# Optimization experiments

Measured on AMD Instinct MI355X. Metric: run time of the kernel, lower is better.

Reference implementation:

```python
import jax, jax.numpy as jnp
import numpy as np

EPS = 1e-8


def setup_inputs() -> dict:
    key = jax.random.key(0)
    ks = jax.random.split(key, 6)
    B, N, d, h = 8, 1024, 512, 512
    features = jax.random.normal(ks[0], (B, N, d), dtype=jnp.float32)
    states_mask = jax.random.randint(ks[1], (B, N), 0, 2, dtype=jnp.int32)
    # nn.Linear params (W stored [out, in], y = x @ W.T + b)
    s1 = 1.0 / np.sqrt(d)
    W1 = jax.random.uniform(ks[2], (h, d), jnp.float32, -s1, s1)
    b1 = jax.random.uniform(ks[3], (h,), jnp.float32, -s1, s1)
    s2 = 1.0 / np.sqrt(3 * h)
    W2 = jax.random.uniform(ks[4], (h, 3 * h), jnp.float32, -s2, s2)
    b2 = jax.random.uniform(ks[5], (h,), jnp.float32, -s2, s2)
    return {"features": features, "states_mask": states_mask,
            "W1": W1, "b1": b1, "W2": W2, "b2": b2}


def reference(features, states_mask, W1, b1, W2, b2):
    B, N, d = features.shape
    # score: project_weight(features) @ features^T  -> [B, N, N]
    proj = features @ W1.T + b1
    weight = jnp.einsum('bid,bjd->bij', proj, features)
    sm = states_mask.astype(jnp.float32)
    mask = sm[:, :, None] * sm[:, None, :]              # [B,N,N]
    tri_past = jnp.tril(jnp.ones((N, N), jnp.float32), k=-1)
    tri_fut = jnp.triu(jnp.ones((N, N), jnp.float32), k=1)
    past_mask = tri_past[None] * mask
    future_mask = tri_fut[None] * mask
    past_w = weight * past_mask
    past_w = past_w / (past_mask.sum(axis=2, keepdims=True) + EPS)
    fut_w = weight * future_mask
    fut_w = fut_w / (future_mask.sum(axis=2, keepdims=True) + EPS)
    # weighted sums: equivalent to the repeated-feature reduction, without O(N^2 d) memory
    past_features = jnp.einsum('bij,bjd->bid', past_w, features)
    future_features = jnp.einsum('bij,bjd->bid', fut_w, features)
    context = jnp.concatenate((past_features, features, future_features), axis=-1)
    context = context @ W2.T + b2
    return context
```

## Files before the change

kernel.cpp:

```cpp
#include <hip/hip_runtime.h>


constexpr int BATCH = 8;
constexpr int SEQ   = 1024;
constexpr int DIM   = 512;
constexpr int HID   = 512;

typedef __bf16 bf16_t;
typedef bf16_t bf16x8 __attribute__((ext_vector_type(8)));
typedef float  f32x4  __attribute__((ext_vector_type(4)));
typedef float  f4     __attribute__((ext_vector_type(4)));

typedef __attribute__((address_space(1))) void gv_t;
typedef __attribute__((address_space(3))) void lv_t;

__device__ __forceinline__ void gload16(const bf16_t* g, bf16_t* l) {
  __builtin_amdgcn_global_load_lds((gv_t*)g, (lv_t*)l, 16, 0, 0);
}

#define WAIT3() asm volatile("s_waitcnt vmcnt(3)" ::: "memory")
#define WAIT0() asm volatile("s_waitcnt vmcnt(0)" ::: "memory")
#define BAR()   { __builtin_amdgcn_s_barrier(); __builtin_amdgcn_sched_barrier(0); }

template <int ROWS>
__device__ __forceinline__ void stage(const bf16_t* g, int ld, bf16_t* lds,
                                      int w, int lane) {
  const int r0 = lane >> 2;
  const int kc = ((((lane & 3) - (lane >> 3)) & 3)) * 8;
#pragma unroll
  for (int i = 0; i < ROWS / 64; ++i) {
    const int s = w * (ROWS / 64) + i;
    gload16(g + (size_t)(s * 16 + r0) * ld + kc, lds + s * 512);
  }
}

__device__ __forceinline__ int swz8(int fr, int c0) {
  return (((fr << 2) | ((c0 + (fr >> 1)) & 3)) << 3);
}

__global__ __launch_bounds__(1024) void scales_kernel(
    const int* __restrict__ smask, float* __restrict__ sp, float* __restrict__ sf) {
  const int b = blockIdx.x, t = threadIdx.x;
  const int v = smask[b * SEQ + t];
  int x = v;
#pragma unroll
  for (int o = 1; o < 64; o <<= 1) {
    int y = __shfl_up(x, o, 64);
    if ((t & 63) >= o) x += y;
  }
  __shared__ int wsum[16], wpre[17];
  if ((t & 63) == 63) wsum[t >> 6] = x;
  __syncthreads();
  if (t == 0) { int c = 0; for (int w = 0; w < 16; ++w) { wpre[w] = c; c += wsum[w]; } wpre[16] = c; }
  __syncthreads();
  const int inc = x + wpre[t >> 6];
  const float P  = (float)(inc - v);
  const float Fu = (float)(wpre[16] - inc);
  sp[b * SEQ + t] = v ? 1.f / (P  + 1e-8f) : 0.f;
  sf[b * SEQ + t] = v ? 1.f / (Fu + 1e-8f) : 0.f;
}

__global__ void cvt_kernel(const float* __restrict__ in, bf16_t* __restrict__ out, int n8) {
  const int i = blockIdx.x * blockDim.x + threadIdx.x;
  if (i >= n8) return;
  const f4* p = (const f4*)(in + (size_t)i * 8);
  f4 v0 = p[0], v1 = p[1];
  bf16x8 o;
  o[0] = (bf16_t)v0[0]; o[1] = (bf16_t)v0[1]; o[2] = (bf16_t)v0[2]; o[3] = (bf16_t)v0[3];
  o[4] = (bf16_t)v1[0]; o[5] = (bf16_t)v1[1]; o[6] = (bf16_t)v1[2]; o[7] = (bf16_t)v1[3];
  *(bf16x8*)(out + (size_t)i * 8) = o;
}

__global__ __launch_bounds__(256) void prepw_kernel(
    const float* __restrict__ W1, const float* __restrict__ W2,
    bf16_t* __restrict__ Wpg, bf16_t* __restrict__ W2ac) {
  const int idx = blockIdx.x * 256 + threadIdx.x;
  const int r = idx >> 6, c8 = (idx & 63) * 8;
  const float* src;
  bf16_t* dst;
  if (r < 512)        { src = W1 + (size_t)r * 512 + c8;                    dst = Wpg  + (size_t)r * 512 + c8; }
  else if (r < 1024)  { src = W2 + (size_t)(r - 512) * 1536 + 512 + c8;     dst = Wpg  + (size_t)r * 512 + c8; }
  else if (r < 1536)  { src = W2 + (size_t)(r - 1024) * 1536 + c8;          dst = W2ac + (size_t)(r - 1024) * 512 + c8; }
  else                { src = W2 + (size_t)(r - 1536) * 1536 + 1024 + c8;   dst = W2ac + (size_t)(r - 1024) * 512 + c8; }
  f4 v0 = *(const f4*)src, v1 = *(const f4*)(src + 4);
  bf16x8 o;
  o[0] = (bf16_t)v0[0]; o[1] = (bf16_t)v0[1]; o[2] = (bf16_t)v0[2]; o[3] = (bf16_t)v0[3];
  o[4] = (bf16_t)v1[0]; o[5] = (bf16_t)v1[1]; o[6] = (bf16_t)v1[2]; o[7] = (bf16_t)v1[3];
  *(bf16x8*)dst = o;
}

__device__ __forceinline__ void gemm_ring(
    const bf16_t* __restrict__ A, int lda, const bf16_t* __restrict__ Bt, int ldb,
    int K, bf16_t* As, bf16_t* Bs, f32x4 acc[4][2],
    int w, int lane, int qoff, int mw, int nw) {
  const int NT = K / 32;
  stage<128>(A,       lda, As,        w, lane);
  stage<64>(Bt,       ldb, Bs,        w, lane);
  stage<128>(A + 32,  lda, As + 4096, w, lane);
  stage<64>(Bt + 32,  ldb, Bs + 2048, w, lane);
  WAIT3();
  BAR();
  int cur = 0;
  for (int k = 0; k < NT; ++k) {
    if (k + 2 < NT) {
      const int nx = (cur >= 1) ? cur - 1 : 2;
      stage<128>(A  + (k + 2) * 32, lda, As + nx * 4096, w, lane);
      stage<64>(Bt + (k + 2) * 32, ldb, Bs + nx * 2048, w, lane);
    }
    const bf16_t* ab = As + cur * 4096 + (mw >> 4) * 512 + qoff;
    const bf16_t* bb = Bs + cur * 2048 + (nw >> 4) * 512 + qoff;
    bf16x8 a[4], b[2];
#pragma unroll
    for (int s = 0; s < 4; ++s) a[s] = *(const bf16x8*)&ab[s * 512];
#pragma unroll
    for (int t = 0; t < 2; ++t) b[t] = *(const bf16x8*)&bb[t * 512];
#pragma unroll
    for (int s = 0; s < 4; ++s)
#pragma unroll
      for (int t = 0; t < 2; ++t)
        acc[s][t] = __builtin_amdgcn_mfma_f32_16x16x32_bf16(a[s], b[t], acc[s][t], 0, 0, 0);
    if (k + 1 < NT) {
      if (k + 2 < NT) { WAIT3(); } else { WAIT0(); }
      BAR();
    }
    cur = (cur == 2) ? 0 : cur + 1;
  }
}

#define TILE_IDS                                  \
  const int tid = threadIdx.x;                    \
  const int w = tid >> 6, lane = tid & 63;        \
  const int fr = lane & 15;                       \
  const int qoff = swz8(fr, lane >> 4);           \
  const int mw = (w >> 1) * 64, nw = (w & 1) * 32;\
  const int cr = (lane >> 4) * 4, cc = lane & 15;

__global__ __launch_bounds__(256) void pg_mfma(
    const bf16_t* __restrict__ Fbf, const bf16_t* __restrict__ Wpg,
    const float* __restrict__ b1, const float* __restrict__ b2,
    bf16_t* __restrict__ projbf, float* __restrict__ out) {
  __shared__ bf16_t As[3 * 4096], Bs[3 * 2048];
  TILE_IDS
  const int m0 = blockIdx.y * 128, n0 = blockIdx.x * 64;
  f32x4 acc[4][2] = {};
  gemm_ring(Fbf + (size_t)m0 * DIM, DIM, Wpg + (size_t)n0 * DIM, DIM, DIM,
            As, Bs, acc, w, lane, qoff, mw, nw);
  if (n0 < 512) {
#pragma unroll
    for (int s = 0; s < 4; ++s)
#pragma unroll
      for (int t = 0; t < 2; ++t) {
        const int col = n0 + nw + t * 16 + cc;
        const float bv = b1[col];
#pragma unroll
        for (int r = 0; r < 4; ++r)
          projbf[(size_t)(m0 + mw + s * 16 + cr + r) * HID + col] = (bf16_t)(acc[s][t][r] + bv);
      }
  } else {
#pragma unroll
    for (int s = 0; s < 4; ++s)
#pragma unroll
      for (int t = 0; t < 2; ++t) {
        const int col = (n0 - 512) + nw + t * 16 + cc;
        const float bv = b2[col];
#pragma unroll
        for (int r = 0; r < 4; ++r)
          out[(size_t)(m0 + mw + s * 16 + cr + r) * HID + col] = acc[s][t][r] + bv;
      }
  }
}

__global__ __launch_bounds__(256) void weight_mfma(
    const bf16_t* __restrict__ projbf, const bf16_t* __restrict__ Fbf,
    bf16_t* __restrict__ wbuf, int b0) {
  __shared__ bf16_t As[3 * 4096], Bs[3 * 2048];
  TILE_IDS
  const int b = b0 + blockIdx.z;
  const bf16_t* A  = projbf + (size_t)b * SEQ * DIM;
  const bf16_t* Bt = Fbf    + (size_t)b * SEQ * DIM;
  bf16_t* C = wbuf + (size_t)blockIdx.z * SEQ * SEQ;
  const int m0 = blockIdx.y * 128, n0 = blockIdx.x * 64;
  f32x4 acc[4][2] = {};
  gemm_ring(A + (size_t)m0 * DIM, DIM, Bt + (size_t)n0 * DIM, DIM, DIM,
            As, Bs, acc, w, lane, qoff, mw, nw);
#pragma unroll
  for (int s = 0; s < 4; ++s)
#pragma unroll
    for (int t = 0; t < 2; ++t)
#pragma unroll
      for (int r = 0; r < 4; ++r)
        C[(size_t)(m0 + mw + s * 16 + cr + r) * SEQ + n0 + nw + t * 16 + cc] = (bf16_t)acc[s][t][r];
}

__global__ __launch_bounds__(256) void gact_mfma(
    const bf16_t* __restrict__ W2ac, const bf16_t* __restrict__ Fbf,
    const int* __restrict__ smask, bf16_t* __restrict__ GacT) {
  __shared__ bf16_t As[3 * 4096], Bs[3 * 2048];
  TILE_IDS
  const int b = blockIdx.z;
  const bf16_t* Bt = Fbf + (size_t)b * SEQ * DIM;
  const int m0 = blockIdx.y * 128, n0 = blockIdx.x * 64;
  f32x4 acc[4][2] = {};
  gemm_ring(W2ac + (size_t)m0 * DIM, DIM, Bt + (size_t)n0 * DIM, DIM, DIM,
            As, Bs, acc, w, lane, qoff, mw, nw);
  bf16_t* C = GacT + (size_t)b * SEQ * SEQ;
#pragma unroll
  for (int s = 0; s < 4; ++s)
#pragma unroll
    for (int t = 0; t < 2; ++t) {
      const int j = n0 + nw + t * 16 + cc;
      const float smj = (float)smask[b * SEQ + j];
#pragma unroll
      for (int r = 0; r < 4; ++r)
        C[(size_t)(m0 + mw + s * 16 + cr + r) * SEQ + j] = (bf16_t)(acc[s][t][r] * smj);
    }
}

__global__ __launch_bounds__(256) void tri_mfma(
    const bf16_t* __restrict__ wbuf, const bf16_t* __restrict__ GacT,
    const float* __restrict__ scaleP, const float* __restrict__ scaleF,
    float* __restrict__ out, int b0) {
  __shared__ bf16_t As[3 * 2048], BPs[3 * 2048], BFs[3 * 2048];
  const int tid = threadIdx.x;
  const int w = tid >> 6, lane = tid & 63;
  const int fr = lane & 15, fk = (lane >> 4) * 8;
  const int qoff = swz8(fr, lane >> 4);
  const int mw = (w >> 1) * 32, nw2 = (w & 1) * 32;
  const int cr = (lane >> 4) * 4, cc = lane & 15;
  const int b = b0 + blockIdx.z;
  const bf16_t* A    = wbuf + (size_t)blockIdx.z * SEQ * SEQ;
  const bf16_t* GaTp = GacT + (size_t)b * SEQ * SEQ + (size_t)(blockIdx.x * 64) * SEQ;
  const bf16_t* GaTf = GaTp + (size_t)512 * SEQ;
  const int i0 = blockIdx.y * 64;
  f32x4 accP[2][2] = {}, accF[2][2] = {};
  const bf16_t* Arow = A + (size_t)i0 * SEQ;
  stage<64>(Arow,      SEQ, As,         w, lane);
  stage<64>(GaTp,      SEQ, BPs,        w, lane);
  stage<64>(GaTf,      SEQ, BFs,        w, lane);
  stage<64>(Arow + 32, SEQ, As + 2048,  w, lane);
  stage<64>(GaTp + 32, SEQ, BPs + 2048, w, lane);
  stage<64>(GaTf + 32, SEQ, BFs + 2048, w, lane);
  WAIT3();
  BAR();
  int cur = 0;
  const int NT = SEQ / 32;
  for (int kt = 0; kt < NT; ++kt) {
    const int j0 = kt * 32;
    if (kt + 2 < NT) {
      const int nx = (cur >= 1) ? cur - 1 : 2;
      const int jn = j0 + 64;
      stage<64>(Arow + jn, SEQ, As  + nx * 2048, w, lane);
      stage<64>(GaTp + jn, SEQ, BPs + nx * 2048, w, lane);
      stage<64>(GaTf + jn, SEQ, BFs + nx * 2048, w, lane);
    }
    const bool wP = (j0 < i0 + mw + 31);
    const bool wF = (j0 + 31 > i0 + mw);
    if (wP || wF) {
      const bf16_t* abase  = As  + cur * 2048 + (mw >> 4) * 512 + qoff;
      const bf16_t* bpbase = BPs + cur * 2048 + (nw2 >> 4) * 512 + qoff;
      const bf16_t* bfbase = BFs + cur * 2048 + (nw2 >> 4) * 512 + qoff;
      bf16x8 bP[2], bF[2];
#pragma unroll
      for (int t = 0; t < 2; ++t) {
        if (wP) bP[t] = *(const bf16x8*)&bpbase[t * 512];
        if (wF) bF[t] = *(const bf16x8*)&bfbase[t * 512];
      }
#pragma unroll
      for (int s = 0; s < 2; ++s) {
        const int rlo = i0 + mw + s * 16;
        const bool pAny = (j0 < rlo + 15), pFull = (j0 + 31 < rlo);
        const bool fAny = (j0 + 31 > rlo), fFull = (j0 > rlo + 15);
        if (!pAny && !fAny) continue;
        const bf16x8 a = *(const bf16x8*)&abase[s * 512];
        if (pFull) {
#pragma unroll
          for (int t = 0; t < 2; ++t)
            accP[s][t] = __builtin_amdgcn_mfma_f32_16x16x32_bf16(a, bP[t], accP[s][t], 0, 0, 0);
        } else if (pAny) {
          const int cut = (rlo + fr) - (j0 + fk);
          bf16x8 ap = a;
#pragma unroll
          for (int e = 0; e < 8; ++e) if (e >= cut) ap[e] = (bf16_t)0.f;
#pragma unroll
          for (int t = 0; t < 2; ++t)
            accP[s][t] = __builtin_amdgcn_mfma_f32_16x16x32_bf16(ap, bP[t], accP[s][t], 0, 0, 0);
        }
        if (fFull) {
#pragma unroll
          for (int t = 0; t < 2; ++t)
            accF[s][t] = __builtin_amdgcn_mfma_f32_16x16x32_bf16(a, bF[t], accF[s][t], 0, 0, 0);
        } else if (fAny) {
          const int cut = (rlo + fr) - (j0 + fk);
          bf16x8 af = a;
#pragma unroll
          for (int e = 0; e < 8; ++e) if (e <= cut) af[e] = (bf16_t)0.f;
#pragma unroll
          for (int t = 0; t < 2; ++t)
            accF[s][t] = __builtin_amdgcn_mfma_f32_16x16x32_bf16(af, bF[t], accF[s][t], 0, 0, 0);
        }
      }
    }
    if (kt + 1 < NT) {
      if (kt + 2 < NT) { WAIT3(); } else { WAIT0(); }
      BAR();
    }
    cur = (cur == 2) ? 0 : cur + 1;
  }
#pragma unroll
  for (int s = 0; s < 2; ++s)
#pragma unroll
    for (int r = 0; r < 4; ++r) {
      const int row = i0 + mw + s * 16 + cr + r;
      const float spv = scaleP[b * SEQ + row];
      const float sfv = scaleF[b * SEQ + row];
#pragma unroll
      for (int t = 0; t < 2; ++t) {
        const int col = blockIdx.x * 64 + nw2 + t * 16 + cc;
        const size_t oi = ((size_t)b * SEQ + row) * HID + col;
        out[oi] = accP[s][t][r] * spv + accF[s][t][r] * sfv + out[oi];
      }
    }
}

extern "C" void kernel_launch(void* const* d_in, const int* in_sizes, int n_in,
                              void* d_out, int out_size, void* d_ws, size_t ws_size,
                              hipStream_t stream) {
  const float* F  = (const float*)d_in[0];
  const int*   sm = (const int*)  d_in[1];
  const float* W1 = (const float*)d_in[2];
  const float* b1 = (const float*)d_in[3];
  const float* W2 = (const float*)d_in[4];
  const float* b2 = (const float*)d_in[5];
  float* out = (float*)d_out;

  char* ws = (char*)d_ws;
  size_t off = 0;
  auto take = [&](size_t bytes) -> void* {
    void* p = ws + off;
    off += (bytes + 255) & ~(size_t)255;
    return p;
  };
  bf16_t* Fbf    = (bf16_t*)take((size_t)BATCH * SEQ * DIM * 2);
  bf16_t* projbf = (bf16_t*)take((size_t)BATCH * SEQ * HID * 2);
  bf16_t* GacT   = (bf16_t*)take((size_t)BATCH * SEQ * SEQ * 2);
  bf16_t* Wpg    = (bf16_t*)take((size_t)1024 * 512 * 2);
  bf16_t* W2ac   = (bf16_t*)take((size_t)1024 * 512 * 2);
  float*  scaleP = (float*) take((size_t)BATCH * SEQ * 4);
  float*  scaleF = (float*) take((size_t)BATCH * SEQ * 4);

  const size_t wbytes = (size_t)SEQ * SEQ * 2;
  int chunk = (ws_size > off) ? (int)((ws_size - off) / wbytes) : 1;
  if (chunk > BATCH) chunk = BATCH;
  if (chunk < 1) chunk = 1;
  bf16_t* wbuf = (bf16_t*)(ws + off);

  scales_kernel<<<dim3(BATCH), dim3(1024), 0, stream>>>(sm, scaleP, scaleF);
  cvt_kernel<<<dim3(BATCH * SEQ * DIM / 8 / 256), dim3(256), 0, stream>>>(F, Fbf, BATCH * SEQ * DIM / 8);
  prepw_kernel<<<dim3(512), dim3(256), 0, stream>>>(W1, W2, Wpg, W2ac);

  pg_mfma<<<dim3(1024 / 64, BATCH * SEQ / 128), dim3(256), 0, stream>>>(
      Fbf, Wpg, b1, b2, projbf, out);
  gact_mfma<<<dim3(SEQ / 64, SEQ / 128, BATCH), dim3(256), 0, stream>>>(
      W2ac, Fbf, sm, GacT);
  for (int b0 = 0; b0 < BATCH; b0 += chunk) {
    const int nb = (BATCH - b0 < chunk) ? (BATCH - b0) : chunk;
    weight_mfma<<<dim3(SEQ / 64, SEQ / 128, nb), dim3(256), 0, stream>>>(projbf, Fbf, wbuf, b0);
    tri_mfma<<<dim3(HID / 64, SEQ / 64, nb), dim3(256), 0, stream>>>(
        wbuf, GacT, scaleP, scaleF, out, b0);
  }
}
```

Before: 107.3 us.

## Merge prep and projection kernels, deepen LDS ring to four stages

New measurement: 121.4 us (median of 2 runs). +13.2%, slower.

```diff
diff --git a/kernel.cpp b/kernel.cpp
--- a/kernel.cpp
+++ b/kernel.cpp
@@ -18,6 +18,7 @@
   __builtin_amdgcn_global_load_lds((gv_t*)g, (lv_t*)l, 16, 0, 0);
 }
 
+#define WAIT6() asm volatile("s_waitcnt vmcnt(6)" ::: "memory")
 #define WAIT3() asm volatile("s_waitcnt vmcnt(3)" ::: "memory")
 #define WAIT0() asm volatile("s_waitcnt vmcnt(0)" ::: "memory")
 #define BAR()   { __builtin_amdgcn_s_barrier(); __builtin_amdgcn_sched_barrier(0); }
@@ -38,55 +39,67 @@
   return (((fr << 2) | ((c0 + (fr >> 1)) & 3)) << 3);
 }
 
-__global__ __launch_bounds__(1024) void scales_kernel(
-    const int* __restrict__ smask, float* __restrict__ sp, float* __restrict__ sf) {
-  const int b = blockIdx.x, t = threadIdx.x;
-  const int v = smask[b * SEQ + t];
-  int x = v;
+__global__ __launch_bounds__(256) void prep_kernel(
+    const float* __restrict__ F, const int* __restrict__ smask,
+    const float* __restrict__ W1, const float* __restrict__ W2,
+    bf16_t* __restrict__ Fbf, bf16_t* __restrict__ Wpg, bf16_t* __restrict__ W2ac,
+    float* __restrict__ sp, float* __restrict__ sf) {
+  const int bid = blockIdx.x, tid = threadIdx.x;
+  if (bid < 2048) {
+    const int i = bid * 256 + tid;
+    const f4* p = (const f4*)(F + (size_t)i * 8);
+    f4 v0 = p[0], v1 = p[1];
+    bf16x8 o;
+    o[0] = (bf16_t)v0[0]; o[1] = (bf16_t)v0[1]; o[2] = (bf16_t)v0[2]; o[3] = (bf16_t)v0[3];
+    o[4] = (bf16_t)v1[0]; o[5] = (bf16_t)v1[1]; o[6] = (bf16_t)v1[2]; o[7] = (bf16_t)v1[3];
+    *(bf16x8*)(Fbf + (size_t)i * 8) = o;
+    return;
+  }
+  if (bid < 2560) {
+    const int idx = (bid - 2048) * 256 + tid;
+    const int r = idx >> 6, c8 = (idx & 63) * 8;
+    const float* src;
+    bf16_t* dst;
+    if (r < 512)       { src = W1 + (size_t)r * 512 + c8;                  dst = Wpg  + (size_t)r * 512 + c8; }
+    else if (r < 1024) { src = W2 + (size_t)(r - 512) * 1536 + 512 + c8;   dst = Wpg  + (size_t)r * 512 + c8; }
+    else if (r < 1536) { src = W2 + (size_t)(r - 1024) * 1536 + c8;        dst = W2ac + (size_t)(r - 1024) * 512 + c8; }
+    else               { src = W2 + (size_t)(r - 1536) * 1536 + 1024 + c8; dst = W2ac + (size_t)(r - 1024) * 512 + c8; }
+    f4 v0 = *(const f4*)src, v1 = *(const f4*)(src + 4);
+    bf16x8 o;
+    o[0] = (bf16_t)v0[0]; o[1] = (bf16_t)v0[1]; o[2] = (bf16_t)v0[2]; o[3] = (bf16_t)v0[3];
+    o[4] = (bf16_t)v1[0]; o[5] = (bf16_t)v1[1]; o[6] = (bf16_t)v1[2]; o[7] = (bf16_t)v1[3];
+    *(bf16x8*)dst = o;
+    return;
+  }
+  const int b = bid - 2560;
+  const int4 v4 = ((const int4*)(smask + b * SEQ))[tid];
+  const int tsum = v4.x + v4.y + v4.z + v4.w;
+  int x = tsum;
 #pragma unroll
   for (int o = 1; o < 64; o <<= 1) {
     int y = __shfl_up(x, o, 64);
-    if ((t & 63) >= o) x += y;
-  }
-  __shared__ int wsum[16], wpre[17];
-  if ((t & 63) == 63) wsum[t >> 6] = x;
+    if ((tid & 63) >= o) x += y;
+  }
+  __shared__ int wsum[4], wpre[5];
+  if ((tid & 63) == 63) wsum[tid >> 6] = x;
   __syncthreads();
-  if (t == 0) { int c = 0; for (int w = 0; w < 16; ++w) { wpre[w] = c; c += wsum[w]; } wpre[16] = c; }
+  if (tid == 0) { int c = 0; for (int w = 0; w < 4; ++w) { wpre[w] = c; c += wsum[w]; } wpre[4] = c; }
   __syncthreads();
-  const int inc = x + wpre[t >> 6];
-  const float P  = (float)(inc - v);
-  const float Fu = (float)(wpre[16] - inc);
-  sp[b * SEQ + t] = v ? 1.f / (P  + 1e-8f) : 0.f;
-  sf[b * SEQ + t] = v ? 1.f / (Fu + 1e-8f) : 0.f;
-}
-
-__global__ void cvt_kernel(const float* __restrict__ in, bf16_t* __restrict__ out, int n8) {
-  const int i = blockIdx.x * blockDim.x + threadIdx.x;
-  if (i >= n8) return;
-  const f4* p = (const f4*)(in + (size_t)i * 8);
-  f4 v0 = p[0], v1 = p[1];
-  bf16x8 o;
-  o[0] = (bf16_t)v0[0]; o[1] = (bf16_t)v0[1]; o[2] = (bf16_t)v0[2]; o[3] = (bf16_t)v0[3];
-  o[4] = (bf16_t)v1[0]; o[5] = (bf16_t)v1[1]; o[6] = (bf16_t)v1[2]; o[7] = (bf16_t)v1[3];
-  *(bf16x8*)(out + (size_t)i * 8) = o;
-}
-
-__global__ __launch_bounds__(256) void prepw_kernel(
-    const float* __restrict__ W1, const float* __restrict__ W2,
-    bf16_t* __restrict__ Wpg, bf16_t* __restrict__ W2ac) {
-  const int idx = blockIdx.x * 256 + threadIdx.x;
-  const int r = idx >> 6, c8 = (idx & 63) * 8;
-  const float* src;
-  bf16_t* dst;
-  if (r < 512)        { src = W1 + (size_t)r * 512 + c8;                    dst = Wpg  + (size_t)r * 512 + c8; }
-  else if (r < 1024)  { src = W2 + (size_t)(r - 512) * 1536 + 512 + c8;     dst = Wpg  + (size_t)r * 512 + c8; }
-  else if (r < 1536)  { src = W2 + (size_t)(r - 1024) * 1536 + c8;          dst = W2ac + (size_t)(r - 1024) * 512 + c8; }
-  else                { src = W2 + (size_t)(r - 1536) * 1536 + 1024 + c8;   dst = W2ac + (size_t)(r - 1024) * 512 + c8; }
-  f4 v0 = *(const f4*)src, v1 = *(const f4*)(src + 4);
-  bf16x8 o;
-  o[0] = (bf16_t)v0[0]; o[1] = (bf16_t)v0[1]; o[2] = (bf16_t)v0[2]; o[3] = (bf16_t)v0[3];
-  o[4] = (bf16_t)v1[0]; o[5] = (bf16_t)v1[1]; o[6] = (bf16_t)v1[2]; o[7] = (bf16_t)v1[3];
-  *(bf16x8*)dst = o;
+  const int excl = (x - tsum) + wpre[tid >> 6];
+  const float tot = (float)wpre[4];
+  f4 spv, sfv;
+  int pre = excl;
+  const int e[4] = {v4.x, v4.y, v4.z, v4.w};
+#pragma unroll
+  for (int i = 0; i < 4; ++i) {
+    const float P  = (float)pre;
+    const float Fu = tot - (float)pre - (float)e[i];
+    spv[i] = e[i] ? 1.f / (P  + 1e-8f) : 0.f;
+    sfv[i] = e[i] ? 1.f / (Fu + 1e-8f) : 0.f;
+    pre += e[i];
+  }
+  ((f4*)(sp + b * SEQ))[tid] = spv;
+  ((f4*)(sf + b * SEQ))[tid] = sfv;
 }
 
 __device__ __forceinline__ void gemm_ring(
@@ -94,18 +107,19 @@
     int K, bf16_t* As, bf16_t* Bs, f32x4 acc[4][2],
     int w, int lane, int qoff, int mw, int nw) {
   const int NT = K / 32;
-  stage<128>(A,       lda, As,        w, lane);
-  stage<64>(Bt,       ldb, Bs,        w, lane);
-  stage<128>(A + 32,  lda, As + 4096, w, lane);
-  stage<64>(Bt + 32,  ldb, Bs + 2048, w, lane);
-  WAIT3();
+#pragma unroll
+  for (int p = 0; p < 3; ++p) {
+    stage<128>(A + p * 32, lda, As + p * 4096, w, lane);
+    stage<64>(Bt + p * 32, ldb, Bs + p * 2048, w, lane);
+  }
+  WAIT6();
   BAR();
-  int cur = 0;
   for (int k = 0; k < NT; ++k) {
-    if (k + 2 < NT) {
-      const int nx = (cur >= 1) ? cur - 1 : 2;
-      stage<128>(A  + (k + 2) * 32, lda, As + nx * 4096, w, lane);
-      stage<64>(Bt + (k + 2) * 32, ldb, Bs + nx * 2048, w, lane);
+    const int cur = k & 3;
+    if (k + 3 < NT) {
+      const int nx = (k + 3) & 3;
+      stage<128>(A  + (k + 3) * 32, lda, As + nx * 4096, w, lane);
+      stage<64>(Bt + (k + 3) * 32, ldb, Bs + nx * 2048, w, lane);
     }
     const bf16_t* ab = As + cur * 4096 + (mw >> 4) * 512 + qoff;
     const bf16_t* bb = Bs + cur * 2048 + (nw >> 4) * 512 + qoff;
@@ -119,53 +133,71 @@
 #pragma unroll
       for (int t = 0; t < 2; ++t)
         acc[s][t] = __builtin_amdgcn_mfma_f32_16x16x32_bf16(a[s], b[t], acc[s][t], 0, 0, 0);
-    if (k + 1 < NT) {
-      if (k + 2 < NT) { WAIT3(); } else { WAIT0(); }
-      BAR();
-    }
-    cur = (cur == 2) ? 0 : cur + 1;
-  }
-}
-
-#define TILE_IDS                                  \
-  const int tid = threadIdx.x;                    \
-  const int w = tid >> 6, lane = tid & 63;        \
-  const int fr = lane & 15;                       \
-  const int qoff = swz8(fr, lane >> 4);           \
-  const int mw = (w >> 1) * 64, nw = (w & 1) * 32;\
+    if (k + 3 < NT)      { WAIT6(); BAR(); }
+    else if (k + 2 < NT) { WAIT3(); BAR(); }
+    else if (k + 1 < NT) { WAIT0(); BAR(); }
+  }
+}
+
+__global__ __launch_bounds__(256) void pgga_mfma(
+    const bf16_t* __restrict__ Fbf, const bf16_t* __restrict__ Wpg,
+    const bf16_t* __restrict__ W2ac, const int* __restrict__ smask,
+    const float* __restrict__ b1, const float* __restrict__ b2,
+    bf16_t* __restrict__ projbf, float* __restrict__ out,
+    bf16_t* __restrict__ GacT) {
+  __shared__ bf16_t As[4 * 4096], Bs[4 * 2048];
+  const int tid = threadIdx.x;
+  const int w = tid >> 6, lane = tid & 63;
+  const int fr = lane & 15;
+  const int qoff = swz8(fr, lane >> 4);
+  const int mw = (w >> 1) * 64, nw = (w & 1) * 32;
   const int cr = (lane >> 4) * 4, cc = lane & 15;
-
-__global__ __launch_bounds__(256) void pg_mfma(
-    const bf16_t* __restrict__ Fbf, const bf16_t* __restrict__ Wpg,
-    const float* __restrict__ b1, const float* __restrict__ b2,
-    bf16_t* __restrict__ projbf, float* __restrict__ out) {
-  __shared__ bf16_t As[3 * 4096], Bs[3 * 2048];
-  TILE_IDS
-  const int m0 = blockIdx.y * 128, n0 = blockIdx.x * 64;
+  const int bid = blockIdx.x;
   f32x4 acc[4][2] = {};
-  gemm_ring(Fbf + (size_t)m0 * DIM, DIM, Wpg + (size_t)n0 * DIM, DIM, DIM,
-            As, Bs, acc, w, lane, qoff, mw, nw);
-  if (n0 < 512) {
+  if (bid < 1024) {
+    const int m0 = (bid >> 4) * 128, n0 = (bid & 15) * 64;
+    gemm_ring(Fbf + (size_t)m0 * DIM, DIM, Wpg + (size_t)n0 * DIM, DIM, DIM,
+              As, Bs, acc, w, lane, qoff, mw, nw);
+    if (n0 < 512) {
+#pragma unroll
+      for (int s = 0; s < 4; ++s)
+#pragma unroll
+        for (int t = 0; t < 2; ++t) {
+          const int col = n0 + nw + t * 16 + cc;
+          const float bv = b1[col];
+#pragma unroll
+          for (int r = 0; r < 4; ++r)
+            projbf[(size_t)(m0 + mw + s * 16 + cr + r) * HID + col] = (bf16_t)(acc[s][t][r] + bv);
+        }
+    } else {
+#pragma unroll
+      for (int s = 0; s < 4; ++s)
+#pragma unroll
+        for (int t = 0; t < 2; ++t) {
+          const int col = (n0 - 512) + nw + t * 16 + cc;
+          const float bv = b2[col];
+#pragma unroll
+          for (int r = 0; r < 4; ++r)
+            out[(size_t)(m0 + mw + s * 16 + cr + r) * HID + col] = acc[s][t][r] + bv;
+        }
+    }
+  } else {
+    const int q = bid - 1024;
+    const int b = q >> 7, r7 = q & 127;
+    const int m0 = (r7 >> 4) * 128, n0 = (r7 & 15) * 64;
+    const bf16_t* Bt = Fbf + (size_t)b * SEQ * DIM;
+    gemm_ring(W2ac + (size_t)m0 * DIM, DIM, Bt + (size_t)n0 * DIM, DIM, DIM,
+              As, Bs, acc, w, lane, qoff, mw, nw);
+    bf16_t* C = GacT + (size_t)b * SEQ * SEQ;
 #pragma unroll
     for (int s = 0; s < 4; ++s)
 #pragma unroll
       for (int t = 0; t < 2; ++t) {
-        const int col = n0 + nw + t * 16 + cc;
-        const float bv = b1[col];
+        const int j = n0 + nw + t * 16 + cc;
+        const float smj = (float)smask[b * SEQ + j];
 #pragma unroll
         for (int r = 0; r < 4; ++r)
-          projbf[(size_t)(m0 + mw + s * 16 + cr + r) * HID + col] = (bf16_t)(acc[s][t][r] + bv);
-      }
-  } else {
-#pragma unroll
-    for (int s = 0; s < 4; ++s)
-#pragma unroll
-      for (int t = 0; t < 2; ++t) {
-        const int col = (n0 - 512) + nw + t * 16 + cc;
-        const float bv = b2[col];
-#pragma unroll
-        for (int r = 0; r < 4; ++r)
-          out[(size_t)(m0 + mw + s * 16 + cr + r) * HID + col] = acc[s][t][r] + bv;
+          C[(size_t)(m0 + mw + s * 16 + cr + r) * SEQ + j] = (bf16_t)(acc[s][t][r] * smj);
       }
   }
 }
@@ -173,8 +205,13 @@
 __global__ __launch_bounds__(256) void weight_mfma(
     const bf16_t* __restrict__ projbf, const bf16_t* __restrict__ Fbf,
     bf16_t* __restrict__ wbuf, int b0) {
-  __shared__ bf16_t As[3 * 4096], Bs[3 * 2048];
-  TILE_IDS
+  __shared__ bf16_t As[4 * 4096], Bs[4 * 2048];
+  const int tid = threadIdx.x;
+  const int w = tid >> 6, lane = tid & 63;
+  const int fr = lane & 15;
+  const int qoff = swz8(fr, lane >> 4);
+  const int mw = (w >> 1) * 64, nw = (w & 1) * 32;
+  const int cr = (lane >> 4) * 4, cc = lane & 15;
   const int b = b0 + blockIdx.z;
   const bf16_t* A  = projbf + (size_t)b * SEQ * DIM;
   const bf16_t* Bt = Fbf    + (size_t)b * SEQ * DIM;
@@ -192,35 +229,11 @@
         C[(size_t)(m0 + mw + s * 16 + cr + r) * SEQ + n0 + nw + t * 16 + cc] = (bf16_t)acc[s][t][r];
 }
 
-__global__ __launch_bounds__(256) void gact_mfma(
-    const bf16_t* __restrict__ W2ac, const bf16_t* __restrict__ Fbf,
-    const int* __restrict__ smask, bf16_t* __restrict__ GacT) {
-  __shared__ bf16_t As[3 * 4096], Bs[3 * 2048];
-  TILE_IDS
-  const int b = blockIdx.z;
-  const bf16_t* Bt = Fbf + (size_t)b * SEQ * DIM;
-  const int m0 = blockIdx.y * 128, n0 = blockIdx.x * 64;
-  f32x4 acc[4][2] = {};
-  gemm_ring(W2ac + (size_t)m0 * DIM, DIM, Bt + (size_t)n0 * DIM, DIM, DIM,
-            As, Bs, acc, w, lane, qoff, mw, nw);
-  bf16_t* C = GacT + (size_t)b * SEQ * SEQ;
-#pragma unroll
-  for (int s = 0; s < 4; ++s)
-#pragma unroll
-    for (int t = 0; t < 2; ++t) {
-      const int j = n0 + nw + t * 16 + cc;
-      const float smj = (float)smask[b * SEQ + j];
-#pragma unroll
-      for (int r = 0; r < 4; ++r)
-        C[(size_t)(m0 + mw + s * 16 + cr + r) * SEQ + j] = (bf16_t)(acc[s][t][r] * smj);
-    }
-}
-
 __global__ __launch_bounds__(256) void tri_mfma(
     const bf16_t* __restrict__ wbuf, const bf16_t* __restrict__ GacT,
     const float* __restrict__ scaleP, const float* __restrict__ scaleF,
     float* __restrict__ out, int b0) {
-  __shared__ bf16_t As[3 * 2048], BPs[3 * 2048], BFs[3 * 2048];
+  __shared__ bf16_t As[4 * 2048], BPs[4 * 2048], BFs[4 * 2048];
   const int tid = threadIdx.x;
   const int w = tid >> 6, lane = tid & 63;
   const int fr = lane & 15, fk = (lane >> 4) * 8;
@@ -234,21 +247,21 @@
   const int i0 = blockIdx.y * 64;
   f32x4 accP[2][2] = {}, accF[2][2] = {};
   const bf16_t* Arow = A + (size_t)i0 * SEQ;
-  stage<64>(Arow,      SEQ, As,         w, lane);
-  stage<64>(GaTp,      SEQ, BPs,        w, lane);
-  stage<64>(GaTf,      SEQ, BFs,        w, lane);
-  stage<64>(Arow + 32, SEQ, As + 2048,  w, lane);
-  stage<64>(GaTp + 32, SEQ, BPs + 2048, w, lane);
-  stage<64>(GaTf + 32, SEQ, BFs + 2048, w, lane);
-  WAIT3();
+#pragma unroll
+  for (int p = 0; p < 3; ++p) {
+    stage<64>(Arow + p * 32, SEQ, As  + p * 2048, w, lane);
+    stage<64>(GaTp + p * 32, SEQ, BPs + p * 2048, w, lane);
+    stage<64>(GaTf + p * 32, SEQ, BFs + p * 2048, w, lane);
+  }
+  WAIT6();
   BAR();
-  int cur = 0;
   const int NT = SEQ / 32;
   for (int kt = 0; kt < NT; ++kt) {
     const int j0 = kt * 32;
-    if (kt + 2 < NT) {
-      const int nx = (cur >= 1) ? cur - 1 : 2;
-      const int jn = j0 + 64;
+    const int cur = kt & 3;
+    if (kt + 3 < NT) {
+      const int nx = (kt + 3) & 3;
+      const int jn = j0 + 96;
       stage<64>(Arow + jn, SEQ, As  + nx * 2048, w, lane);
       stage<64>(GaTp + jn, SEQ, BPs + nx * 2048, w, lane);
       stage<64>(GaTf + jn, SEQ, BFs + nx * 2048, w, lane);
@@ -300,11 +313,9 @@
         }
       }
     }
-    if (kt + 1 < NT) {
-      if (kt + 2 < NT) { WAIT3(); } else { WAIT0(); }
-      BAR();
-    }
-    cur = (cur == 2) ? 0 : cur + 1;
+    if (kt + 3 < NT)      { WAIT6(); BAR(); }
+    else if (kt + 2 < NT) { WAIT3(); BAR(); }
+    else if (kt + 1 < NT) { WAIT0(); BAR(); }
   }
 #pragma unroll
   for (int s = 0; s < 2; ++s)
@@ -354,14 +365,10 @@
   if (chunk < 1) chunk = 1;
   bf16_t* wbuf = (bf16_t*)(ws + off);
 
-  scales_kernel<<<dim3(BATCH), dim3(1024), 0, stream>>>(sm, scaleP, scaleF);
-  cvt_kernel<<<dim3(BATCH * SEQ * DIM / 8 / 256), dim3(256), 0, stream>>>(F, Fbf, BATCH * SEQ * DIM / 8);
-  prepw_kernel<<<dim3(512), dim3(256), 0, stream>>>(W1, W2, Wpg, W2ac);
-
-  pg_mfma<<<dim3(1024 / 64, BATCH * SEQ / 128), dim3(256), 0, stream>>>(
-      Fbf, Wpg, b1, b2, projbf, out);
-  gact_mfma<<<dim3(SEQ / 64, SEQ / 128, BATCH), dim3(256), 0, stream>>>(
-      W2ac, Fbf, sm, GacT);
+  prep_kernel<<<dim3(2568), dim3(256), 0, stream>>>(
+      F, sm, W1, W2, Fbf, Wpg, W2ac, scaleP, scaleF);
+  pgga_mfma<<<dim3(2048), dim3(256), 0, stream>>>(
+      Fbf, Wpg, W2ac, sm, b1, b2, projbf, out, GacT);
   for (int b0 = 0; b0 < BATCH; b0 += chunk) {
     const int nb = (BATCH - b0 < chunk) ? (BATCH - b0) : chunk;
     weight_mfma<<<dim3(SEQ / 64, SEQ / 128, nb), dim3(256), 0, stream>>>(projbf, Fbf, wbuf, b0);
```
